# Optimization experiments

Measured on AMD Instinct MI355X. Metric: run time of the kernel, lower is better.

The kernel has to match this reference:

```python
import jax, jax.numpy as jnp
import numpy as np

B, S, H, C = 16, 4096, 1024, 64

def setup_inputs() -> dict:
    key = jax.random.key(0)
    k1, k2 = jax.random.split(key)
    hidden = jax.random.normal(k1, (B, S, H), dtype=jnp.float32)
    querys = jax.random.normal(k2, (C, H), dtype=jnp.float32)
    return {"hidden": hidden, "querys": querys}

def reference(hidden, querys):
    # scores: [B, C, S] = einsum over hidden_size
    scores = jnp.einsum('bsh,ch->bcs', hidden, querys)
    # softmax over the sequence axis
    factor = jax.nn.softmax(scores, axis=2)
    # pooled: [B, C, H]
    result = jnp.einsum('bcs,bsh->bch', factor, hidden)
    # flatten to [B, C*H]
    return result.reshape(-1, querys.shape[0] * querys.shape[1])
```

## Files before the change

kernel.cpp:

```cpp
#include <hip/hip_runtime.h>
#include <math.h>

#define BB 16
#define SS 4096
#define HH 1024
#define CC 64

typedef __attribute__((ext_vector_type(4))) float f32x4;
typedef __attribute__((ext_vector_type(8))) short s16x8;

__device__ __forceinline__ ushort f2bf(float x) {
    union { float f; unsigned u; } un; un.f = x;
    unsigned r = (un.u + 0x7FFFu + ((un.u >> 16) & 1u)) >> 16;
    return (ushort)r;
}
__device__ __forceinline__ float bf2f(ushort h) {
    union { unsigned u; float f; } un; un.u = ((unsigned)h) << 16; return un.f;
}

__global__ __launch_bounds__(256) void prep_querys_kernel(
    const float* __restrict__ q, ushort* __restrict__ qhi, ushort* __restrict__ qlo)
{
    const int i4 = blockIdx.x * 256 + threadIdx.x;
    const float4 v = ((const float4*)q)[i4];
    ushort4 h, l;
    h.x = f2bf(v.x); l.x = f2bf(v.x - bf2f(h.x));
    h.y = f2bf(v.y); l.y = f2bf(v.y - bf2f(h.y));
    h.z = f2bf(v.z); l.z = f2bf(v.z - bf2f(h.z));
    h.w = f2bf(v.w); l.w = f2bf(v.w - bf2f(h.w));
    ((ushort4*)qhi)[i4] = h;
    ((ushort4*)qlo)[i4] = l;
}

__global__ __launch_bounds__(256) void scores_kernel(
    const float* __restrict__ hidden, const ushort* __restrict__ qhi,
    const ushort* __restrict__ qlo, float* __restrict__ scores)
{
    __shared__ __align__(16) ushort Ahi[128][40];
    __shared__ __align__(16) ushort Alo[128][40];
    __shared__ __align__(16) ushort Bhi[64][40];
    __shared__ __align__(16) ushort Blo[64][40];

    const int b  = blockIdx.y;
    const int s0 = blockIdx.x * 128;
    const int t  = threadIdx.x;
    const int w    = t >> 6;
    const int lane = t & 63;
    const int col  = lane & 15;
    const int quad = lane >> 4;
    const int lr = t >> 3;
    const int lc = t & 7;

    f32x4 acc[2][4];
#pragma unroll
    for (int i = 0; i < 2; ++i)
#pragma unroll
        for (int j = 0; j < 4; ++j) acc[i][j] = (f32x4){0.f, 0.f, 0.f, 0.f};

    const float* hbase = hidden + ((size_t)b * SS + s0) * HH;

    float4 hv[4];
    ushort4 qh[2], ql[2];
#pragma unroll
    for (int p = 0; p < 4; ++p)
        hv[p] = *(const float4*)&hbase[(size_t)(lr + 32 * p) * HH + lc * 4];
#pragma unroll
    for (int p = 0; p < 2; ++p) {
        qh[p] = ((const ushort4*)qhi)[(lr + 32 * p) * 256 + lc];
        ql[p] = ((const ushort4*)qlo)[(lr + 32 * p) * 256 + lc];
    }

    for (int k0 = 0; k0 < HH; k0 += 32) {
        __syncthreads();
#pragma unroll
        for (int p = 0; p < 4; ++p) {
            const int r = lr + 32 * p;
            ushort4 h, l;
            h.x = f2bf(hv[p].x); l.x = f2bf(hv[p].x - bf2f(h.x));
            h.y = f2bf(hv[p].y); l.y = f2bf(hv[p].y - bf2f(h.y));
            h.z = f2bf(hv[p].z); l.z = f2bf(hv[p].z - bf2f(h.z));
            h.w = f2bf(hv[p].w); l.w = f2bf(hv[p].w - bf2f(h.w));
            *(ushort4*)&Ahi[r][lc * 4] = h;
            *(ushort4*)&Alo[r][lc * 4] = l;
        }
#pragma unroll
        for (int p = 0; p < 2; ++p) {
            *(ushort4*)&Bhi[lr + 32 * p][lc * 4] = qh[p];
            *(ushort4*)&Blo[lr + 32 * p][lc * 4] = ql[p];
        }
        __syncthreads();

        if (k0 + 32 < HH) {
            const int kn = k0 + 32;
#pragma unroll
            for (int p = 0; p < 4; ++p)
                hv[p] = *(const float4*)&hbase[(size_t)(lr + 32 * p) * HH + kn + lc * 4];
#pragma unroll
            for (int p = 0; p < 2; ++p) {
                qh[p] = ((const ushort4*)qhi)[(lr + 32 * p) * 256 + kn / 4 + lc];
                ql[p] = ((const ushort4*)qlo)[(lr + 32 * p) * 256 + kn / 4 + lc];
            }
        }

        s16x8 ah[2], al[2], bh[4], bl[4];
#pragma unroll
        for (int mt = 0; mt < 2; ++mt) {
            const int r = w * 32 + mt * 16 + col;
            ah[mt] = *(const s16x8*)&Ahi[r][quad * 8];
            al[mt] = *(const s16x8*)&Alo[r][quad * 8];
        }
#pragma unroll
        for (int nt = 0; nt < 4; ++nt) {
            const int r = nt * 16 + col;
            bh[nt] = *(const s16x8*)&Bhi[r][quad * 8];
            bl[nt] = *(const s16x8*)&Blo[r][quad * 8];
        }
#pragma unroll
        for (int mt = 0; mt < 2; ++mt)
#pragma unroll
            for (int nt = 0; nt < 4; ++nt) {
                acc[mt][nt] = __builtin_amdgcn_mfma_f32_16x16x32_bf16(ah[mt], bh[nt], acc[mt][nt], 0, 0, 0);
                acc[mt][nt] = __builtin_amdgcn_mfma_f32_16x16x32_bf16(ah[mt], bl[nt], acc[mt][nt], 0, 0, 0);
                acc[mt][nt] = __builtin_amdgcn_mfma_f32_16x16x32_bf16(al[mt], bh[nt], acc[mt][nt], 0, 0, 0);
            }
    }

#pragma unroll
    for (int mt = 0; mt < 2; ++mt)
#pragma unroll
        for (int nt = 0; nt < 4; ++nt) {
            const int c = nt * 16 + col;
            const int s = s0 + w * 32 + mt * 16 + quad * 4;
            *(f32x4*)&scores[((size_t)(b * CC + c)) * SS + s] = acc[mt][nt];
        }
}

__global__ __launch_bounds__(256) void softmax_kernel(
    const float* __restrict__ scores, ushort* __restrict__ factor)
{
    const float* p = scores + (size_t)blockIdx.x * SS;
    ushort* f = factor + (size_t)blockIdx.x * SS;
    const int t = threadIdx.x;
    float4 v[4];
    float m = -3.0e38f;
#pragma unroll
    for (int i = 0; i < 4; ++i) {
        v[i] = *(const float4*)&p[t * 4 + i * 1024];
        m = fmaxf(m, fmaxf(fmaxf(v[i].x, v[i].y), fmaxf(v[i].z, v[i].w)));
    }
#pragma unroll
    for (int off = 1; off < 64; off <<= 1) m = fmaxf(m, __shfl_xor(m, off));
    __shared__ float redm[4];
    __shared__ float reds[4];
    const int wave = t >> 6, lane = t & 63;
    if (lane == 0) redm[wave] = m;
    __syncthreads();
    m = fmaxf(fmaxf(redm[0], redm[1]), fmaxf(redm[2], redm[3]));

    float sum = 0.0f;
#pragma unroll
    for (int i = 0; i < 4; ++i) {
        v[i].x = __expf(v[i].x - m); v[i].y = __expf(v[i].y - m);
        v[i].z = __expf(v[i].z - m); v[i].w = __expf(v[i].w - m);
        sum += (v[i].x + v[i].y) + (v[i].z + v[i].w);
    }
#pragma unroll
    for (int off = 1; off < 64; off <<= 1) sum += __shfl_xor(sum, off);
    if (lane == 0) reds[wave] = sum;
    __syncthreads();
    sum = (reds[0] + reds[1]) + (reds[2] + reds[3]);
    const float inv = 1.0f / sum;
#pragma unroll
    for (int i = 0; i < 4; ++i) {
        ushort4 o;
        o.x = f2bf(v[i].x * inv); o.y = f2bf(v[i].y * inv);
        o.z = f2bf(v[i].z * inv); o.w = f2bf(v[i].w * inv);
        ((ushort4*)f)[t + i * 256] = o;
    }
}

__global__ __launch_bounds__(256) void pool_kernel(
    const float* __restrict__ hidden, const ushort* __restrict__ factor,
    float* __restrict__ parts)
{
    __shared__ __align__(16) ushort Ht[64][72];

    const int b  = blockIdx.y;
    const int h0 = blockIdx.x * 64;
    const int ks = blockIdx.z;
    const int sbeg = ks * (SS / 4);
    const int t = threadIdx.x;
    const int w = t >> 6, lane = t & 63, col = lane & 15, quad = lane >> 4;
    const int hc = t & 15;
    const int sq = t >> 4;

    f32x4 acc[4];
#pragma unroll
    for (int j = 0; j < 4; ++j) acc[j] = (f32x4){0.f, 0.f, 0.f, 0.f};

    const float* hbase = hidden + (size_t)b * SS * HH + h0;
    const ushort* fbase = factor + (size_t)(b * CC + w * 16 + col) * SS + sbeg;

    float v[16];
#pragma unroll
    for (int pp = 0; pp < 2; ++pp)
#pragma unroll
        for (int mm = 0; mm < 4; ++mm)
#pragma unroll
            for (int e = 0; e < 2; ++e)
                v[pp * 8 + mm * 2 + e] =
                    hbase[(size_t)(sbeg + 2 * (sq + 16 * pp) + e) * HH + hc + 16 * mm];

    for (int sc = 0; sc < SS / 4; sc += 64) {
        __syncthreads();
#pragma unroll
        for (int pp = 0; pp < 2; ++pp)
#pragma unroll
            for (int mm = 0; mm < 4; ++mm) {
                unsigned pack = (unsigned)f2bf(v[pp * 8 + mm * 2 + 0]) |
                                ((unsigned)f2bf(v[pp * 8 + mm * 2 + 1]) << 16);
                ((unsigned*)Ht)[(hc + 16 * mm) * 36 + (sq + 16 * pp)] = pack;
            }
        __syncthreads();

        const s16x8 fa0 = *(const s16x8*)&fbase[sc + quad * 8];
        const s16x8 fa1 = *(const s16x8*)&fbase[sc + 32 + quad * 8];

        if (sc + 64 < SS / 4) {
#pragma unroll
            for (int pp = 0; pp < 2; ++pp)
#pragma unroll
                for (int mm = 0; mm < 4; ++mm)
#pragma unroll
                    for (int e = 0; e < 2; ++e)
                        v[pp * 8 + mm * 2 + e] =
                            hbase[(size_t)(sbeg + sc + 64 + 2 * (sq + 16 * pp) + e) * HH + hc + 16 * mm];
        }

#pragma unroll
        for (int ksp = 0; ksp < 2; ++ksp) {
            const s16x8 fa = ksp ? fa1 : fa0;
#pragma unroll
            for (int nt = 0; nt < 4; ++nt) {
                const s16x8 hb = *(const s16x8*)&Ht[nt * 16 + col][ksp * 32 + quad * 8];
                acc[nt] = __builtin_amdgcn_mfma_f32_16x16x32_bf16(fa, hb, acc[nt], 0, 0, 0);
            }
        }
    }

    float* dst = parts + (size_t)ks * (BB * CC * HH) + (size_t)b * (CC * HH);
#pragma unroll
    for (int nt = 0; nt < 4; ++nt) {
        const int h = h0 + nt * 16 + col;
#pragma unroll
        for (int r = 0; r < 4; ++r) {
            const int c = w * 16 + quad * 4 + r;
            dst[(size_t)c * HH + h] = acc[nt][r];
        }
    }
}

__global__ __launch_bounds__(256) void reduce4_kernel(
    const float* __restrict__ parts, float* __restrict__ out)
{
    const int i = blockIdx.x * 256 + threadIdx.x;
    const float4* p = (const float4*)parts;
    const float4 a = p[i];
    const float4 b = p[i + 262144];
    const float4 c = p[i + 524288];
    const float4 d = p[i + 786432];
    float4 r;
    r.x = (a.x + b.x) + (c.x + d.x);
    r.y = (a.y + b.y) + (c.y + d.y);
    r.z = (a.z + b.z) + (c.z + d.z);
    r.w = (a.w + b.w) + (c.w + d.w);
    ((float4*)out)[i] = r;
}

extern "C" void kernel_launch(void* const* d_in, const int* in_sizes, int n_in,
                              void* d_out, int out_size, void* d_ws, size_t ws_size,
                              hipStream_t stream)
{
    const float* hidden = (const float*)d_in[0];
    const float* querys = (const float*)d_in[1];
    float* out = (float*)d_out;

    float*  scores = (float*)d_ws;
    float*  parts  = (float*)d_ws;
    ushort* factor = (ushort*)((char*)d_ws + (16u << 20));
    ushort* qhi    = (ushort*)((char*)d_ws + (24u << 20));
    ushort* qlo    = qhi + CC * HH;

    prep_querys_kernel<<<dim3(CC * HH / 1024), 256, 0, stream>>>(querys, qhi, qlo);
    scores_kernel<<<dim3(SS / 128, BB), 256, 0, stream>>>(hidden, qhi, qlo, scores);
    softmax_kernel<<<dim3(BB * CC), 256, 0, stream>>>(scores, factor);
    pool_kernel<<<dim3(HH / 64, BB, 4), 256, 0, stream>>>(hidden, factor, parts);
    reduce4_kernel<<<dim3(1024), 256, 0, stream>>>(parts, out);
}
```

Measured before the change: 455.6 us.

## Drop LDS staging in scores kernel and split pool reduction eightfold

The scores kernel no longer stages data in shared memory. Each wave loads its own 16 hidden rows straight from global memory into MFMA operand registers and reads the query hi/lo tiles directly from global or cache. This removes the barriers and LDS traffic, and the grid doubles to 64-row blocks. The pool kernel's sequence split goes from 4 to 8 to expose more parallelism, the reduction kernel now sums 8 partials, and the partials buffer moves to its own workspace region, which needs more workspace and adds reduce traffic.

```diff
diff --git a/kernel.cpp b/kernel.cpp
--- a/kernel.cpp
+++ b/kernel.cpp
@@ -36,103 +36,52 @@
     const float* __restrict__ hidden, const ushort* __restrict__ qhi,
     const ushort* __restrict__ qlo, float* __restrict__ scores)
 {
-    __shared__ __align__(16) ushort Ahi[128][40];
-    __shared__ __align__(16) ushort Alo[128][40];
-    __shared__ __align__(16) ushort Bhi[64][40];
-    __shared__ __align__(16) ushort Blo[64][40];
-
-    const int b  = blockIdx.y;
-    const int s0 = blockIdx.x * 128;
-    const int t  = threadIdx.x;
-    const int w    = t >> 6;
-    const int lane = t & 63;
-    const int col  = lane & 15;
-    const int quad = lane >> 4;
-    const int lr = t >> 3;
-    const int lc = t & 7;
-
-    f32x4 acc[2][4];
-#pragma unroll
-    for (int i = 0; i < 2; ++i)
-#pragma unroll
-        for (int j = 0; j < 4; ++j) acc[i][j] = (f32x4){0.f, 0.f, 0.f, 0.f};
-
-    const float* hbase = hidden + ((size_t)b * SS + s0) * HH;
-
-    float4 hv[4];
-    ushort4 qh[2], ql[2];
-#pragma unroll
-    for (int p = 0; p < 4; ++p)
-        hv[p] = *(const float4*)&hbase[(size_t)(lr + 32 * p) * HH + lc * 4];
-#pragma unroll
-    for (int p = 0; p < 2; ++p) {
-        qh[p] = ((const ushort4*)qhi)[(lr + 32 * p) * 256 + lc];
-        ql[p] = ((const ushort4*)qlo)[(lr + 32 * p) * 256 + lc];
-    }
+    const int b = blockIdx.y, t = threadIdx.x;
+    const int w = t >> 6, lane = t & 63, col = lane & 15, quad = lane >> 4;
+    const int s0 = blockIdx.x * 64 + w * 16;
+
+    const float*  arow = hidden + ((size_t)b * SS + s0 + col) * HH + quad * 8;
+    const ushort* qh0  = qhi + (size_t)col * HH + quad * 8;
+    const ushort* ql0  = qlo + (size_t)col * HH + quad * 8;
+
+    f32x4 acc[4];
+#pragma unroll
+    for (int nt = 0; nt < 4; ++nt) acc[nt] = (f32x4){0.f, 0.f, 0.f, 0.f};
+
+    float4 a0 = *(const float4*)arow;
+    float4 a1 = *(const float4*)(arow + 4);
 
     for (int k0 = 0; k0 < HH; k0 += 32) {
-        __syncthreads();
-#pragma unroll
-        for (int p = 0; p < 4; ++p) {
-            const int r = lr + 32 * p;
-            ushort4 h, l;
-            h.x = f2bf(hv[p].x); l.x = f2bf(hv[p].x - bf2f(h.x));
-            h.y = f2bf(hv[p].y); l.y = f2bf(hv[p].y - bf2f(h.y));
-            h.z = f2bf(hv[p].z); l.z = f2bf(hv[p].z - bf2f(h.z));
-            h.w = f2bf(hv[p].w); l.w = f2bf(hv[p].w - bf2f(h.w));
-            *(ushort4*)&Ahi[r][lc * 4] = h;
-            *(ushort4*)&Alo[r][lc * 4] = l;
-        }
-#pragma unroll
-        for (int p = 0; p < 2; ++p) {
-            *(ushort4*)&Bhi[lr + 32 * p][lc * 4] = qh[p];
-            *(ushort4*)&Blo[lr + 32 * p][lc * 4] = ql[p];
-        }
-        __syncthreads();
-
+        s16x8 bh[4], bl[4];
+#pragma unroll
+        for (int nt = 0; nt < 4; ++nt) {
+            bh[nt] = *(const s16x8*)(qh0 + (size_t)nt * 16 * HH + k0);
+            bl[nt] = *(const s16x8*)(ql0 + (size_t)nt * 16 * HH + k0);
+        }
+        const float af[8] = {a0.x, a0.y, a0.z, a0.w, a1.x, a1.y, a1.z, a1.w};
+        s16x8 ah, al;
+#pragma unroll
+        for (int j = 0; j < 8; ++j) {
+            const ushort h = f2bf(af[j]);
+            ah[j] = (short)h;
+            al[j] = (short)f2bf(af[j] - bf2f(h));
+        }
         if (k0 + 32 < HH) {
-            const int kn = k0 + 32;
-#pragma unroll
-            for (int p = 0; p < 4; ++p)
-                hv[p] = *(const float4*)&hbase[(size_t)(lr + 32 * p) * HH + kn + lc * 4];
-#pragma unroll
-            for (int p = 0; p < 2; ++p) {
-                qh[p] = ((const ushort4*)qhi)[(lr + 32 * p) * 256 + kn / 4 + lc];
-                ql[p] = ((const ushort4*)qlo)[(lr + 32 * p) * 256 + kn / 4 + lc];
-            }
-        }
-
-        s16x8 ah[2], al[2], bh[4], bl[4];
-#pragma unroll
-        for (int mt = 0; mt < 2; ++mt) {
-            const int r = w * 32 + mt * 16 + col;
-            ah[mt] = *(const s16x8*)&Ahi[r][quad * 8];
-            al[mt] = *(const s16x8*)&Alo[r][quad * 8];
+            a0 = *(const float4*)(arow + k0 + 32);
+            a1 = *(const float4*)(arow + k0 + 36);
         }
 #pragma unroll
         for (int nt = 0; nt < 4; ++nt) {
-            const int r = nt * 16 + col;
-            bh[nt] = *(const s16x8*)&Bhi[r][quad * 8];
-            bl[nt] = *(const s16x8*)&Blo[r][quad * 8];
-        }
-#pragma unroll
-        for (int mt = 0; mt < 2; ++mt)
-#pragma unroll
-            for (int nt = 0; nt < 4; ++nt) {
-                acc[mt][nt] = __builtin_amdgcn_mfma_f32_16x16x32_bf16(ah[mt], bh[nt], acc[mt][nt], 0, 0, 0);
-                acc[mt][nt] = __builtin_amdgcn_mfma_f32_16x16x32_bf16(ah[mt], bl[nt], acc[mt][nt], 0, 0, 0);
-                acc[mt][nt] = __builtin_amdgcn_mfma_f32_16x16x32_bf16(al[mt], bh[nt], acc[mt][nt], 0, 0, 0);
-            }
-    }
-
-#pragma unroll
-    for (int mt = 0; mt < 2; ++mt)
-#pragma unroll
-        for (int nt = 0; nt < 4; ++nt) {
-            const int c = nt * 16 + col;
-            const int s = s0 + w * 32 + mt * 16 + quad * 4;
-            *(f32x4*)&scores[((size_t)(b * CC + c)) * SS + s] = acc[mt][nt];
-        }
+            acc[nt] = __builtin_amdgcn_mfma_f32_16x16x32_bf16(ah, bh[nt], acc[nt], 0, 0, 0);
+            acc[nt] = __builtin_amdgcn_mfma_f32_16x16x32_bf16(ah, bl[nt], acc[nt], 0, 0, 0);
+            acc[nt] = __builtin_amdgcn_mfma_f32_16x16x32_bf16(al, bh[nt], acc[nt], 0, 0, 0);
+        }
+    }
+#pragma unroll
+    for (int nt = 0; nt < 4; ++nt) {
+        const int c = nt * 16 + col;
+        *(f32x4*)&scores[((size_t)(b * CC + c)) * SS + s0 + quad * 4] = acc[nt];
+    }
 }
 
 __global__ __launch_bounds__(256) void softmax_kernel(
@@ -179,6 +128,7 @@
     }
 }
 
+#define KSPLIT 8
 __global__ __launch_bounds__(256) void pool_kernel(
     const float* __restrict__ hidden, const ushort* __restrict__ factor,
     float* __restrict__ parts)
@@ -188,7 +138,7 @@
     const int b  = blockIdx.y;
     const int h0 = blockIdx.x * 64;
     const int ks = blockIdx.z;
-    const int sbeg = ks * (SS / 4);
+    const int sbeg = ks * (SS / KSPLIT);
     const int t = threadIdx.x;
     const int w = t >> 6, lane = t & 63, col = lane & 15, quad = lane >> 4;
     const int hc = t & 15;
@@ -211,7 +161,7 @@
                 v[pp * 8 + mm * 2 + e] =
                     hbase[(size_t)(sbeg + 2 * (sq + 16 * pp) + e) * HH + hc + 16 * mm];
 
-    for (int sc = 0; sc < SS / 4; sc += 64) {
+    for (int sc = 0; sc < SS / KSPLIT; sc += 64) {
         __syncthreads();
 #pragma unroll
         for (int pp = 0; pp < 2; ++pp)
@@ -226,7 +176,7 @@
         const s16x8 fa0 = *(const s16x8*)&fbase[sc + quad * 8];
         const s16x8 fa1 = *(const s16x8*)&fbase[sc + 32 + quad * 8];
 
-        if (sc + 64 < SS / 4) {
+        if (sc + 64 < SS / KSPLIT) {
 #pragma unroll
             for (int pp = 0; pp < 2; ++pp)
 #pragma unroll
@@ -260,20 +210,17 @@
     }
 }
 
-__global__ __launch_bounds__(256) void reduce4_kernel(
+__global__ __launch_bounds__(256) void reduce8_kernel(
     const float* __restrict__ parts, float* __restrict__ out)
 {
     const int i = blockIdx.x * 256 + threadIdx.x;
     const float4* p = (const float4*)parts;
-    const float4 a = p[i];
-    const float4 b = p[i + 262144];
-    const float4 c = p[i + 524288];
-    const float4 d = p[i + 786432];
-    float4 r;
-    r.x = (a.x + b.x) + (c.x + d.x);
-    r.y = (a.y + b.y) + (c.y + d.y);
-    r.z = (a.z + b.z) + (c.z + d.z);
-    r.w = (a.w + b.w) + (c.w + d.w);
+    float4 r = {0.f, 0.f, 0.f, 0.f};
+#pragma unroll
+    for (int j = 0; j < KSPLIT; ++j) {
+        const float4 a = p[i + (size_t)j * 262144];
+        r.x += a.x; r.y += a.y; r.z += a.z; r.w += a.w;
+    }
     ((float4*)out)[i] = r;
 }
 
@@ -286,14 +233,14 @@
     float* out = (float*)d_out;
 
     float*  scores = (float*)d_ws;
-    float*  parts  = (float*)d_ws;
     ushort* factor = (ushort*)((char*)d_ws + (16u << 20));
     ushort* qhi    = (ushort*)((char*)d_ws + (24u << 20));
     ushort* qlo    = qhi + CC * HH;
+    float*  parts  = (float*)((char*)d_ws + (32u << 20));
 
     prep_querys_kernel<<<dim3(CC * HH / 1024), 256, 0, stream>>>(querys, qhi, qlo);
-    scores_kernel<<<dim3(SS / 128, BB), 256, 0, stream>>>(hidden, qhi, qlo, scores);
+    scores_kernel<<<dim3(SS / 64, BB), 256, 0, stream>>>(hidden, qhi, qlo, scores);
     softmax_kernel<<<dim3(BB * CC), 256, 0, stream>>>(scores, factor);
-    pool_kernel<<<dim3(HH / 64, BB, 4), 256, 0, stream>>>(hidden, factor, parts);
-    reduce4_kernel<<<dim3(1024), 256, 0, stream>>>(parts, out);
-}
+    pool_kernel<<<dim3(HH / 64, BB, KSPLIT), 256, 0, stream>>>(hidden, factor, parts);
+    reduce8_kernel<<<dim3(1024), 256, 0, stream>>>(parts, out);
+}
```

After: 502.6 us. +10.3%, slower.
